# Kernel tuning notes

Hardware: AMD Instinct MI355X
Metric: run time of the kernel (lower is better)

Reference implementation:

```python
import jax, jax.numpy as jnp
import numpy as np

NUM_HEADS = 8
DIM_HEAD = 32
WINDOW = 8
SHIFT = 4
C = NUM_HEADS * DIM_HEAD  # 256


def _relative_position_index(w):
    coords = np.stack(np.meshgrid(np.arange(w), np.arange(w), indexing='ij'))  # [2,w,w]
    cf = coords.reshape(2, -1)                       # [2, w*w]
    rel = cf[:, :, None] - cf[:, None, :]            # [2, N, N]
    rel = rel.transpose(1, 2, 0) + (w - 1)           # [N, N, 2]
    rel = rel * np.array([2 * w - 1, 1])
    return rel.sum(-1)                               # [N, N] int

REL_IDX = jnp.asarray(_relative_position_index(WINDOW))  # [64,64]


def setup_inputs() -> dict:
    key = jax.random.key(0)
    ks = jax.random.split(key, 4)
    B, H, W = 4, 256, 256
    x = jax.random.normal(ks[0], (B, H, W, C), dtype=jnp.float32)
    w_qkv = jax.random.normal(ks[1], (C, 3 * C), dtype=jnp.float32) * 0.02
    b_qkv = jnp.zeros((3 * C,), dtype=jnp.float32)
    w_proj = jax.random.normal(ks[2], (C, C), dtype=jnp.float32) * 0.02
    b_proj = jnp.zeros((C,), dtype=jnp.float32)
    bias_table = jax.random.normal(ks[3], ((2 * WINDOW - 1) ** 2, NUM_HEADS), dtype=jnp.float32) * 0.02
    return {"x": x, "w_qkv": w_qkv, "b_qkv": b_qkv, "w_proj": w_proj, "b_proj": b_proj, "bias_table": bias_table}


def _window_partition(x, w):
    B, H, W_, Ch = x.shape
    x = x.reshape(B, H // w, w, W_ // w, w, Ch)
    x = x.transpose(0, 1, 3, 2, 4, 5)
    return x.reshape(-1, w, w, Ch)


def _window_reverse(windows, w, H, W_):
    Ch = windows.shape[-1]
    x = windows.reshape(-1, H // w, W_ // w, w, w, Ch)
    x = x.transpose(0, 1, 3, 2, 4, 5)
    return x.reshape(-1, H, W_, Ch)


def reference(x, w_qkv, b_qkv, w_proj, b_proj, bias_table):
    B, H, W_, Ch = x.shape
    N = WINDOW * WINDOW
    shifted = jnp.roll(x, (-SHIFT, -SHIFT), axis=(1, 2)) if SHIFT > 0 else x
    xw = _window_partition(shifted, WINDOW).reshape(-1, N, Ch)   # [nWB, 64, C]
    qkv = xw @ w_qkv + b_qkv                                      # [nWB, 64, 3C]
    qkv = qkv.reshape(-1, N, 3, NUM_HEADS, DIM_HEAD).transpose(2, 0, 3, 1, 4)
    q, k, v = qkv[0], qkv[1], qkv[2]                              # [nWB, h, 64, d]
    q = q * (DIM_HEAD ** -0.5)
    attn = jnp.einsum('whnd,whmd->whnm', q, k)                    # [nWB, h, 64, 64]
    rel_bias = bias_table[REL_IDX.reshape(-1)].reshape(N, N, NUM_HEADS).transpose(2, 0, 1)
    attn = jax.nn.softmax(attn + rel_bias, axis=-1)
    out = jnp.einsum('whnm,whmd->whnd', attn, v)                  # [nWB, h, 64, d]
    out = out.transpose(0, 2, 1, 3).reshape(-1, WINDOW, WINDOW, Ch)
    shifted_out = _window_reverse(out, WINDOW, H, W_)
    y = jnp.roll(shifted_out, (SHIFT, SHIFT), axis=(1, 2)) if SHIFT > 0 else shifted_out
    return y @ w_proj + b_proj
```

## Files before the change

### kernel.cpp

```cpp
#include <hip/hip_runtime.h>

typedef __attribute__((ext_vector_type(8))) short bf16x8;
typedef __attribute__((ext_vector_type(4))) float f32x4;

#define MFMA(a, b, c) __builtin_amdgcn_mfma_f32_16x16x32_bf16(a, b, c, 0, 0, 0)

__device__ __forceinline__ unsigned int pack2(float x, float y) {
  union { float f; unsigned u; } a{x}, b{y};
  unsigned ax = a.u + 0x7FFFu + ((a.u >> 16) & 1u);
  unsigned bx = b.u + 0x7FFFu + ((b.u >> 16) & 1u);
  return (ax >> 16) | (bx & 0xFFFF0000u);
}
__device__ __forceinline__ unsigned short f2bf(float x) {
  union { float f; unsigned u; } a{x};
  unsigned r = a.u + 0x7FFFu + ((a.u >> 16) & 1u);
  return (unsigned short)(r >> 16);
}
__device__ __forceinline__ bf16x8 pack8(f32x4 a, f32x4 b) {
  union { unsigned u[4]; bf16x8 v; } r;
  r.u[0] = pack2(a[0], a[1]); r.u[1] = pack2(a[2], a[3]);
  r.u[2] = pack2(b[0], b[1]); r.u[3] = pack2(b[2], b[3]);
  return r.v;
}

__device__ __forceinline__ int src_off(int t) {
  int wi = t >> 6, n = t & 63;
  int b = wi >> 10, wr = (wi >> 5) & 31, wc = wi & 31;
  int hh = (wr * 8 + (n >> 3) + 4) & 255;
  int ww = (wc * 8 + (n & 7) + 4) & 255;
  return ((((b << 8) | hh) << 8) | ww) << 8;
}

__global__ __launch_bounds__(256) void prep_kernel(
    const float* __restrict__ w_qkv, const float* __restrict__ w_proj,
    const float* __restrict__ bias_table,
    unsigned short* __restrict__ wqkvt, unsigned short* __restrict__ wpt,
    float* __restrict__ rb2) {
  int i = blockIdx.x * 256 + threadIdx.x;
  if (i < 196608) {
    wqkvt[i] = f2bf(w_qkv[(i & 255) * 768 + (i >> 8)]);
  } else if (i < 262144) {
    int j = i - 196608;
    wpt[j] = f2bf(w_proj[(j & 255) * 256 + (j >> 8)]);
  } else {
    int j = i - 262144;
    int jr = j & 3, ln = (j >> 2) & 15, g = (j >> 6) & 3;
    int nt = (j >> 8) & 3, mt = (j >> 10) & 3, h = j >> 12;
    int q = 16 * nt + ln;
    int k = 16 * mt + 4 * g + jr;
    int idx = ((q >> 3) - (k >> 3) + 7) * 15 + ((q & 7) - (k & 7) + 7);
    rb2[j] = bias_table[idx * 8 + h];
  }
}

__global__ __launch_bounds__(512, 4) void fused_kernel(
    const float* __restrict__ x, const unsigned short* __restrict__ wqkvt,
    const float* __restrict__ b_qkv, const unsigned short* __restrict__ wpt,
    const float* __restrict__ b_proj, const float* __restrict__ rb2,
    float* __restrict__ y) {
  __shared__ unsigned short sm[36864];
  int wi = blockIdx.x;
  int tid = threadIdx.x;
  int h = tid >> 6, lane = tid & 63, ln = lane & 15, g = lane >> 4;
  unsigned short* R1 = sm + 16384 + h * 2560;

  int tb = wi * 64;
  {
    int tok0 = tid >> 4, ck = tid & 15;
    int tok1 = tok0 + 32;
    const float4* s0 = (const float4*)(x + src_off(tb + tok0) + ck * 16);
    const float4* s1 = (const float4*)(x + src_off(tb + tok1) + ck * 16);
    float4 a0 = s0[0], a1 = s0[1], a2 = s0[2], a3 = s0[3];
    float4 b0 = s1[0], b1 = s1[1], b2 = s1[2], b3 = s1[3];
    uint4 w0, w1;
    w0.x = pack2(a0.x, a0.y); w0.y = pack2(a0.z, a0.w);
    w0.z = pack2(a1.x, a1.y); w0.w = pack2(a1.z, a1.w);
    w1.x = pack2(a2.x, a2.y); w1.y = pack2(a2.z, a2.w);
    w1.z = pack2(a3.x, a3.y); w1.w = pack2(a3.z, a3.w);
    int base0 = tok0 * 512 + ck * 32, swz0 = (tok0 & 7) << 4;
    *(uint4*)((char*)sm + ((base0) ^ swz0)) = w0;
    *(uint4*)((char*)sm + ((base0 + 16) ^ swz0)) = w1;
    w0.x = pack2(b0.x, b0.y); w0.y = pack2(b0.z, b0.w);
    w0.z = pack2(b1.x, b1.y); w0.w = pack2(b1.z, b1.w);
    w1.x = pack2(b2.x, b2.y); w1.y = pack2(b2.z, b2.w);
    w1.z = pack2(b3.x, b3.y); w1.w = pack2(b3.z, b3.w);
    int base1 = tok1 * 512 + ck * 32, swz1 = (tok1 & 7) << 4;
    *(uint4*)((char*)sm + ((base1) ^ swz1)) = w0;
    *(uint4*)((char*)sm + ((base1 + 16) ^ swz1)) = w1;
  }
  __syncthreads();

  {
    f32x4 av[4][2] = {};
#pragma unroll 2
    for (int ks = 0; ks < 8; ++ks) {
      bf16x8 xf[4];
#pragma unroll
      for (int t = 0; t < 4; ++t) {
        int row = 16 * t + ln;
        xf[t] = *(const bf16x8*)((char*)sm + ((row * 512 + ks * 64 + 16 * g) ^ ((row & 7) << 4)));
      }
      bf16x8 wv[2];
#pragma unroll
      for (int dt = 0; dt < 2; ++dt)
        wv[dt] = *(const bf16x8*)(wqkvt + (512 + 32 * h + 16 * dt + ln) * 256 + ks * 32 + 8 * g);
#pragma unroll
      for (int mt = 0; mt < 4; ++mt)
#pragma unroll
        for (int dt = 0; dt < 2; ++dt)
          av[mt][dt] = MFMA(xf[mt], wv[dt], av[mt][dt]);
    }
#pragma unroll
    for (int dt = 0; dt < 2; ++dt) {
      float bv_ = b_qkv[512 + 32 * h + 16 * dt + ln];
#pragma unroll
      for (int mt = 0; mt < 4; ++mt) {
        ushort4 vp;
        vp.x = f2bf(av[mt][dt][0] + bv_); vp.y = f2bf(av[mt][dt][1] + bv_);
        vp.z = f2bf(av[mt][dt][2] + bv_); vp.w = f2bf(av[mt][dt][3] + bv_);
        *(ushort4*)&R1[(16 * dt + ln) * 72 + 32 * (mt >> 1) + 8 * g + 4 * (mt & 1)] = vp;
      }
    }
  }

  bf16x8 qf[4], kf[4];
  {
    f32x4 accq[2][4] = {}, acck[2][4] = {};
    int nr0 = (32 * h + ln) * 256 + 8 * g;
    int nr1 = (32 * h + 16 + ln) * 256 + 8 * g;
    bf16x8 cwq[2], cwk[2];
    cwq[0] = *(const bf16x8*)(wqkvt + nr0);
    cwq[1] = *(const bf16x8*)(wqkvt + nr1);
    cwk[0] = *(const bf16x8*)(wqkvt + 65536 + nr0);
    cwk[1] = *(const bf16x8*)(wqkvt + 65536 + nr1);
#pragma unroll 1
    for (int ks = 0; ks < 8; ++ks) {
      int kn = ((ks + 1) & 7) * 32;
      bf16x8 nwq[2], nwk[2];
      nwq[0] = *(const bf16x8*)(wqkvt + nr0 + kn);
      nwq[1] = *(const bf16x8*)(wqkvt + nr1 + kn);
      nwk[0] = *(const bf16x8*)(wqkvt + 65536 + nr0 + kn);
      nwk[1] = *(const bf16x8*)(wqkvt + 65536 + nr1 + kn);
      bf16x8 xf[4];
#pragma unroll
      for (int t = 0; t < 4; ++t) {
        int row = 16 * t + ln;
        xf[t] = *(const bf16x8*)((char*)sm + ((row * 512 + ks * 64 + 16 * g) ^ ((row & 7) << 4)));
      }
#pragma unroll
      for (int mt = 0; mt < 2; ++mt)
#pragma unroll
        for (int nt = 0; nt < 4; ++nt) {
          accq[mt][nt] = MFMA(cwq[mt], xf[nt], accq[mt][nt]);
          acck[mt][nt] = MFMA(cwk[mt], xf[nt], acck[mt][nt]);
        }
      cwq[0] = nwq[0]; cwq[1] = nwq[1];
      cwk[0] = nwk[0]; cwk[1] = nwk[1];
    }
    f32x4 bq0 = *(const f32x4*)(b_qkv + 32 * h + 4 * g);
    f32x4 bq1 = *(const f32x4*)(b_qkv + 32 * h + 16 + 4 * g);
    f32x4 bk0 = *(const f32x4*)(b_qkv + 256 + 32 * h + 4 * g);
    f32x4 bk1 = *(const f32x4*)(b_qkv + 256 + 32 * h + 16 + 4 * g);
    const float sc = 0.17677669529663687f;
#pragma unroll
    for (int nt = 0; nt < 4; ++nt) {
      qf[nt] = pack8((accq[0][nt] + bq0) * sc, (accq[1][nt] + bq1) * sc);
      kf[nt] = pack8(acck[0][nt] + bk0, acck[1][nt] + bk1);
    }
  }

  f32x4 st[4][4];
  const float* rbw = rb2 + h * 4096;
#pragma unroll
  for (int mt = 0; mt < 4; ++mt)
#pragma unroll
    for (int nt = 0; nt < 4; ++nt)
      st[mt][nt] = *(const f32x4*)(rbw + ((((mt * 4 + nt) * 4 + g) * 16 + ln) * 4));
#pragma unroll
  for (int mt = 0; mt < 4; ++mt)
#pragma unroll
    for (int nt = 0; nt < 4; ++nt)
      st[mt][nt] = MFMA(kf[mt], qf[nt], st[mt][nt]);

  bf16x8 vf[2][2];
#pragma unroll
  for (int kk = 0; kk < 2; ++kk)
#pragma unroll
    for (int nd = 0; nd < 2; ++nd)
      vf[kk][nd] = *(const bf16x8*)&R1[(16 * nd + ln) * 72 + 32 * kk + 8 * g];

  bf16x8 pb[2][4];
#pragma unroll
  for (int nt = 0; nt < 4; ++nt) {
    float mx = st[0][nt][0];
#pragma unroll
    for (int mt = 0; mt < 4; ++mt)
#pragma unroll
      for (int jr = 0; jr < 4; ++jr) mx = fmaxf(mx, st[mt][nt][jr]);
    mx = fmaxf(mx, __shfl_xor(mx, 16));
    mx = fmaxf(mx, __shfl_xor(mx, 32));
    float sum = 0.f;
#pragma unroll
    for (int mt = 0; mt < 4; ++mt)
#pragma unroll
      for (int jr = 0; jr < 4; ++jr) {
        float p = __expf(st[mt][nt][jr] - mx);
        st[mt][nt][jr] = p; sum += p;
      }
    sum += __shfl_xor(sum, 16);
    sum += __shfl_xor(sum, 32);
    float inv = 1.f / sum;
    pb[0][nt] = pack8(st[0][nt] * inv, st[1][nt] * inv);
    pb[1][nt] = pack8(st[2][nt] * inv, st[3][nt] * inv);
  }

  f32x4 o[2][4] = {};
#pragma unroll
  for (int kk = 0; kk < 2; ++kk)
#pragma unroll
    for (int dt = 0; dt < 2; ++dt)
#pragma unroll
      for (int nt = 0; nt < 4; ++nt)
        o[dt][nt] = MFMA(vf[kk][dt], pb[kk][nt], o[dt][nt]);

#pragma unroll
  for (int dt = 0; dt < 2; ++dt)
#pragma unroll
    for (int nt = 0; nt < 4; ++nt) {
      uint2 vp;
      vp.x = pack2(o[dt][nt][0], o[dt][nt][1]);
      vp.y = pack2(o[dt][nt][2], o[dt][nt][3]);
      *(uint2*)&R1[(16 * nt + ln) * 40 + 16 * dt + 4 * g] = vp;
    }
  __syncthreads();

  f32x4 a2[4][2] = {};
#pragma unroll 2
  for (int ks = 0; ks < 8; ++ks) {
    const unsigned short* AO = sm + 16384 + ks * 2560;
    bf16x8 af2[4], bf2[2];
#pragma unroll
    for (int mt = 0; mt < 4; ++mt)
      af2[mt] = *(const bf16x8*)&AO[(16 * mt + ln) * 40 + 8 * g];
#pragma unroll
    for (int nt = 0; nt < 2; ++nt)
      bf2[nt] = *(const bf16x8*)(wpt + (32 * h + 16 * nt + ln) * 256 + ks * 32 + 8 * g);
#pragma unroll
    for (int mt = 0; mt < 4; ++mt) {
      a2[mt][0] = MFMA(af2[mt], bf2[0], a2[mt][0]);
      a2[mt][1] = MFMA(af2[mt], bf2[1], a2[mt][1]);
    }
  }
  int b = wi >> 10, wr = (wi >> 5) & 31, wc = wi & 31;
  int hb = wr * 8 + (g >> 1) + 4;
  int wb = wc * 8 + 4 * (g & 1) + 4;
  int colb = 32 * h + ln;
  float bp0 = b_proj[colb], bp1 = b_proj[colb + 16];
#pragma unroll
  for (int mt = 0; mt < 4; ++mt) {
    int hh = (hb + 2 * mt) & 255;
#pragma unroll
    for (int jr = 0; jr < 4; ++jr) {
      int ww = (wb + jr) & 255;
      float* yp = y + (((((b << 8) | hh) << 8) | ww) << 8) + colb;
      yp[0]  = a2[mt][0][jr] + bp0;
      yp[16] = a2[mt][1][jr] + bp1;
    }
  }
}

extern "C" void kernel_launch(void* const* d_in, const int* in_sizes, int n_in,
                              void* d_out, int out_size, void* d_ws, size_t ws_size,
                              hipStream_t stream) {
  const float* x          = (const float*)d_in[0];
  const float* w_qkv      = (const float*)d_in[1];
  const float* b_qkv      = (const float*)d_in[2];
  const float* w_proj     = (const float*)d_in[3];
  const float* b_proj     = (const float*)d_in[4];
  const float* bias_table = (const float*)d_in[5];
  char* ws = (char*)d_ws;
  unsigned short* wqkvt = (unsigned short*)(ws);
  unsigned short* wpt   = (unsigned short*)(ws + 393216);
  float* rb2            = (float*)(ws + 524288);
  float* y = (float*)d_out;

  prep_kernel<<<1152, 256, 0, stream>>>(w_qkv, w_proj, bias_table, wqkvt, wpt, rb2);
  fused_kernel<<<4096, 512, 0, stream>>>(x, wqkvt, b_qkv, wpt, b_proj, rb2, y);
}
```

Measured before the change: 333.3 us.

## Use hardware bf16 conversion, add MFMA priority hints, drop Q/K weight prefetch, restructure softmax

Replaces the manual round-to-nearest bf16 packing with native __bf16 conversions, which can map to hardware packed-convert instructions. Wraps every MFMA block in s_setprio raise/lower so waves issuing matrix ops get scheduling priority. Removes the software double-buffered prefetch of the Q/K weights in favour of in-loop loads, and restructures the softmax max/sum reductions as tree reductions for more instruction-level parallelism. The prefetch removal may expose global load latency, and the new conversion may round NaN or edge cases differently.

```diff
diff --git a/kernel.cpp b/kernel.cpp
--- a/kernel.cpp
+++ b/kernel.cpp
@@ -1,15 +1,18 @@
 #include <hip/hip_runtime.h>
+#include <hip/hip_bf16.h>
 
 typedef __attribute__((ext_vector_type(8))) short bf16x8;
 typedef __attribute__((ext_vector_type(4))) float f32x4;
+typedef __attribute__((ext_vector_type(2))) __bf16 bf16x2t;
 
 #define MFMA(a, b, c) __builtin_amdgcn_mfma_f32_16x16x32_bf16(a, b, c, 0, 0, 0)
 
 __device__ __forceinline__ unsigned int pack2(float x, float y) {
-  union { float f; unsigned u; } a{x}, b{y};
-  unsigned ax = a.u + 0x7FFFu + ((a.u >> 16) & 1u);
-  unsigned bx = b.u + 0x7FFFu + ((b.u >> 16) & 1u);
-  return (ax >> 16) | (bx & 0xFFFF0000u);
+  bf16x2t v;
+  v.x = (__bf16)x; v.y = (__bf16)y;
+  union { bf16x2t v; unsigned u; } c;
+  c.v = v;
+  return c.u;
 }
 __device__ __forceinline__ unsigned short f2bf(float x) {
   union { float f; unsigned u; } a{x};
@@ -104,21 +107,23 @@
 #pragma unroll
       for (int dt = 0; dt < 2; ++dt)
         wv[dt] = *(const bf16x8*)(wqkvt + (512 + 32 * h + 16 * dt + ln) * 256 + ks * 32 + 8 * g);
+      __builtin_amdgcn_s_setprio(1);
 #pragma unroll
       for (int mt = 0; mt < 4; ++mt)
 #pragma unroll
         for (int dt = 0; dt < 2; ++dt)
           av[mt][dt] = MFMA(xf[mt], wv[dt], av[mt][dt]);
+      __builtin_amdgcn_s_setprio(0);
     }
 #pragma unroll
     for (int dt = 0; dt < 2; ++dt) {
       float bv_ = b_qkv[512 + 32 * h + 16 * dt + ln];
 #pragma unroll
       for (int mt = 0; mt < 4; ++mt) {
-        ushort4 vp;
-        vp.x = f2bf(av[mt][dt][0] + bv_); vp.y = f2bf(av[mt][dt][1] + bv_);
-        vp.z = f2bf(av[mt][dt][2] + bv_); vp.w = f2bf(av[mt][dt][3] + bv_);
-        *(ushort4*)&R1[(16 * dt + ln) * 72 + 32 * (mt >> 1) + 8 * g + 4 * (mt & 1)] = vp;
+        uint2 vp;
+        vp.x = pack2(av[mt][dt][0] + bv_, av[mt][dt][1] + bv_);
+        vp.y = pack2(av[mt][dt][2] + bv_, av[mt][dt][3] + bv_);
+        *(uint2*)&R1[(16 * dt + ln) * 72 + 32 * (mt >> 1) + 8 * g + 4 * (mt & 1)] = vp;
       }
     }
   }
@@ -126,36 +131,30 @@
   bf16x8 qf[4], kf[4];
   {
     f32x4 accq[2][4] = {}, acck[2][4] = {};
-    int nr0 = (32 * h + ln) * 256 + 8 * g;
-    int nr1 = (32 * h + 16 + ln) * 256 + 8 * g;
-    bf16x8 cwq[2], cwk[2];
-    cwq[0] = *(const bf16x8*)(wqkvt + nr0);
-    cwq[1] = *(const bf16x8*)(wqkvt + nr1);
-    cwk[0] = *(const bf16x8*)(wqkvt + 65536 + nr0);
-    cwk[1] = *(const bf16x8*)(wqkvt + 65536 + nr1);
 #pragma unroll 1
     for (int ks = 0; ks < 8; ++ks) {
-      int kn = ((ks + 1) & 7) * 32;
-      bf16x8 nwq[2], nwk[2];
-      nwq[0] = *(const bf16x8*)(wqkvt + nr0 + kn);
-      nwq[1] = *(const bf16x8*)(wqkvt + nr1 + kn);
-      nwk[0] = *(const bf16x8*)(wqkvt + 65536 + nr0 + kn);
-      nwk[1] = *(const bf16x8*)(wqkvt + 65536 + nr1 + kn);
       bf16x8 xf[4];
 #pragma unroll
       for (int t = 0; t < 4; ++t) {
         int row = 16 * t + ln;
         xf[t] = *(const bf16x8*)((char*)sm + ((row * 512 + ks * 64 + 16 * g) ^ ((row & 7) << 4)));
       }
+      bf16x8 wq[2], wk[2];
+#pragma unroll
+      for (int mt = 0; mt < 2; ++mt) {
+        int nr = 32 * h + 16 * mt + ln;
+        wq[mt] = *(const bf16x8*)(wqkvt + nr * 256 + ks * 32 + 8 * g);
+        wk[mt] = *(const bf16x8*)(wqkvt + (256 + nr) * 256 + ks * 32 + 8 * g);
+      }
+      __builtin_amdgcn_s_setprio(1);
 #pragma unroll
       for (int mt = 0; mt < 2; ++mt)
 #pragma unroll
         for (int nt = 0; nt < 4; ++nt) {
-          accq[mt][nt] = MFMA(cwq[mt], xf[nt], accq[mt][nt]);
-          acck[mt][nt] = MFMA(cwk[mt], xf[nt], acck[mt][nt]);
+          accq[mt][nt] = MFMA(wq[mt], xf[nt], accq[mt][nt]);
+          acck[mt][nt] = MFMA(wk[mt], xf[nt], acck[mt][nt]);
         }
-      cwq[0] = nwq[0]; cwq[1] = nwq[1];
-      cwk[0] = nwk[0]; cwk[1] = nwk[1];
+      __builtin_amdgcn_s_setprio(0);
     }
     f32x4 bq0 = *(const f32x4*)(b_qkv + 32 * h + 4 * g);
     f32x4 bq1 = *(const f32x4*)(b_qkv + 32 * h + 16 + 4 * g);
@@ -176,11 +175,13 @@
 #pragma unroll
     for (int nt = 0; nt < 4; ++nt)
       st[mt][nt] = *(const f32x4*)(rbw + ((((mt * 4 + nt) * 4 + g) * 16 + ln) * 4));
+  __builtin_amdgcn_s_setprio(1);
 #pragma unroll
   for (int mt = 0; mt < 4; ++mt)
 #pragma unroll
     for (int nt = 0; nt < 4; ++nt)
       st[mt][nt] = MFMA(kf[mt], qf[nt], st[mt][nt]);
+  __builtin_amdgcn_s_setprio(0);
 
   bf16x8 vf[2][2];
 #pragma unroll
@@ -192,29 +193,36 @@
   bf16x8 pb[2][4];
 #pragma unroll
   for (int nt = 0; nt < 4; ++nt) {
-    float mx = st[0][nt][0];
-#pragma unroll
-    for (int mt = 0; mt < 4; ++mt)
-#pragma unroll
-      for (int jr = 0; jr < 4; ++jr) mx = fmaxf(mx, st[mt][nt][jr]);
+    f32x4 ma, mb;
+#pragma unroll
+    for (int jr = 0; jr < 4; ++jr) {
+      ma[jr] = fmaxf(st[0][nt][jr], st[1][nt][jr]);
+      mb[jr] = fmaxf(st[2][nt][jr], st[3][nt][jr]);
+    }
+    float mx = fmaxf(fmaxf(fmaxf(ma[0], mb[0]), fmaxf(ma[1], mb[1])),
+                     fmaxf(fmaxf(ma[2], mb[2]), fmaxf(ma[3], mb[3])));
     mx = fmaxf(mx, __shfl_xor(mx, 16));
     mx = fmaxf(mx, __shfl_xor(mx, 32));
-    float sum = 0.f;
-#pragma unroll
-    for (int mt = 0; mt < 4; ++mt)
-#pragma unroll
-      for (int jr = 0; jr < 4; ++jr) {
-        float p = __expf(st[mt][nt][jr] - mx);
-        st[mt][nt][jr] = p; sum += p;
-      }
+    f32x4 e0, e1, e2, e3;
+#pragma unroll
+    for (int jr = 0; jr < 4; ++jr) {
+      e0[jr] = __expf(st[0][nt][jr] - mx);
+      e1[jr] = __expf(st[1][nt][jr] - mx);
+      e2[jr] = __expf(st[2][nt][jr] - mx);
+      e3[jr] = __expf(st[3][nt][jr] - mx);
+    }
+    f32x4 s01 = e0 + e1, s23 = e2 + e3;
+    float sum = (s01[0] + s23[0]) + (s01[1] + s23[1])
+              + ((s01[2] + s23[2]) + (s01[3] + s23[3]));
     sum += __shfl_xor(sum, 16);
     sum += __shfl_xor(sum, 32);
     float inv = 1.f / sum;
-    pb[0][nt] = pack8(st[0][nt] * inv, st[1][nt] * inv);
-    pb[1][nt] = pack8(st[2][nt] * inv, st[3][nt] * inv);
+    pb[0][nt] = pack8(e0 * inv, e1 * inv);
+    pb[1][nt] = pack8(e2 * inv, e3 * inv);
   }
 
   f32x4 o[2][4] = {};
+  __builtin_amdgcn_s_setprio(1);
 #pragma unroll
   for (int kk = 0; kk < 2; ++kk)
 #pragma unroll
@@ -222,6 +230,7 @@
 #pragma unroll
       for (int nt = 0; nt < 4; ++nt)
         o[dt][nt] = MFMA(vf[kk][dt], pb[kk][nt], o[dt][nt]);
+  __builtin_amdgcn_s_setprio(0);
 
 #pragma unroll
   for (int dt = 0; dt < 2; ++dt)
@@ -245,11 +254,13 @@
 #pragma unroll
     for (int nt = 0; nt < 2; ++nt)
       bf2[nt] = *(const bf16x8*)(wpt + (32 * h + 16 * nt + ln) * 256 + ks * 32 + 8 * g);
+    __builtin_amdgcn_s_setprio(1);
 #pragma unroll
     for (int mt = 0; mt < 4; ++mt) {
       a2[mt][0] = MFMA(af2[mt], bf2[0], a2[mt][0]);
       a2[mt][1] = MFMA(af2[mt], bf2[1], a2[mt][1]);
     }
+    __builtin_amdgcn_s_setprio(0);
   }
   int b = wi >> 10, wr = (wi >> 5) & 31, wc = wi & 31;
   int hb = wr * 8 + (g >> 1) + 4;
```

Result: no change. 337.9 us (+1.4%).
